# Kernel tuning notes

Hardware: AMD Instinct MI355X
Metric: run time of the kernel (lower is better)

The kernel has to match this reference:

```python
import jax, jax.numpy as jnp
import numpy as np

EPS = 1e-6
NUM_HEADS = 8
FOCUS = 3.0


def setup_inputs() -> dict:
    key = jax.random.key(0)
    ks = jax.random.split(key, 8)
    B, N, C = 16, 4096, 256
    head_dim, ksz = C // NUM_HEADS, 5
    s = 1.0 / np.sqrt(C)
    return {
        "x": jax.random.normal(ks[0], (B, N, C), jnp.float32),
        "Wq": jax.random.normal(ks[1], (C, C), jnp.float32) * s,
        "Wkv": jax.random.normal(ks[2], (C, 2 * C), jnp.float32) * s,
        "Wp": jax.random.normal(ks[3], (C, C), jnp.float32) * s,
        "bp": jnp.zeros((C,), jnp.float32),
        "scale_param": jnp.zeros((1, 1, C), jnp.float32),
        "pos_enc": jax.random.normal(ks[4], (1, N, C), jnp.float32) * 0.02,
        "dwc_w": jax.random.normal(ks[5], (head_dim, 1, ksz, ksz), jnp.float32) * 0.1,
        "dwc_b": jnp.zeros((head_dim,), jnp.float32),
        "H": 64,
        "W": 64,
    }


def _focus(t, scale, f):
    # relu feature map + power focusing with norm restoration
    t = (jax.nn.relu(t) + EPS) / scale
    tn = jnp.linalg.norm(t, axis=-1, keepdims=True)
    tf = t ** f
    return tf / jnp.linalg.norm(tf, axis=-1, keepdims=True) * tn


def reference(x, Wq, Wkv, Wp, bp, scale_param, pos_enc, dwc_w, dwc_b, H, W):
    B, N, C = x.shape
    h = NUM_HEADS
    d = C // h
    n = N  # sr_ratio == 1

    q = x @ Wq                                  # [B,N,C]
    kv = x @ Wkv                                # [B,N,2C]
    k, v = kv[..., :C], kv[..., C:]
    k = k + pos_enc

    scale = jax.nn.softplus(scale_param)
    q = _focus(q, scale, FOCUS)
    k = _focus(k, scale, FOCUS)

    # split heads: [B,h,N,d]
    qh = q.reshape(B, N, h, d).transpose(0, 2, 1, 3)
    kh = k.reshape(B, n, h, d).transpose(0, 2, 1, 3)
    vh = v.reshape(B, n, h, d).transpose(0, 2, 1, 3)

    # linear attention: z = 1/(q . mean_n(k)), kv = k^T v / n, out = (q @ kv) * z
    z = 1.0 / (jnp.einsum("bhnd,bhd->bhn", qh, kh.mean(axis=2)) + EPS)
    kvmat = jnp.einsum("bhnd,bhne->bhde", kh, vh) / n     # [B,h,d,d]
    out = jnp.einsum("bhnd,bhde->bhne", qh, kvmat) * z[..., None]

    out = out.transpose(0, 2, 1, 3).reshape(B, N, C)      # [B,N,C]

    # depthwise conv on v over the HxW grid, per head-channel
    v4 = vh.reshape(B * h, H, W, d).transpose(0, 3, 1, 2)  # [B*h,d,H,W]
    conv = jax.lax.conv_general_dilated(
        v4, dwc_w, window_strides=(1, 1), padding="SAME",
        feature_group_count=d,
        dimension_numbers=("NCHW", "OIHW", "NCHW"))
    conv = conv + dwc_b[None, :, None, None]
    out = out + conv.reshape(B, C, N).transpose(0, 2, 1)

    return out @ Wp + bp
```

## Files before the change

### kernel.cpp

```cpp
#include <hip/hip_runtime.h>
#include <hip/hip_bf16.h>

typedef unsigned short u16;
using bf16_t = __hip_bfloat16;
typedef short short8 __attribute__((ext_vector_type(8)));
typedef float f32x4 __attribute__((ext_vector_type(4)));

__device__ __forceinline__ float b2f(u16 u) {
    return __uint_as_float((unsigned int)u << 16);
}
__device__ __forceinline__ u16 f2b(float f) {
    bf16_t h = __float2bfloat16(f);
    union { bf16_t h; u16 u; } cv; cv.h = h; return cv.u;
}
__device__ __forceinline__ float ldv(const void* p, size_t i, int f32) {
    return f32 ? ((const float*)p)[i] : b2f(((const u16*)p)[i]);
}
__device__ __forceinline__ uint4 pack8(float4 a, float4 b) {
    uint4 u;
    u.x = (unsigned)f2b(a.x) | ((unsigned)f2b(a.y) << 16);
    u.y = (unsigned)f2b(a.z) | ((unsigned)f2b(a.w) << 16);
    u.z = (unsigned)f2b(b.x) | ((unsigned)f2b(b.y) << 16);
    u.w = (unsigned)f2b(b.z) | ((unsigned)f2b(b.w) << 16);
    return u;
}
__device__ __forceinline__ int swz(int n, int k) {
    return k ^ ((n & 7) << 3);
}
__device__ __forceinline__ void gl16(const u16* g, u16* l) {
    __builtin_amdgcn_global_load_lds(
        (const __attribute__((address_space(1))) unsigned int*)g,
        (__attribute__((address_space(3))) unsigned int*)l, 16, 0, 0);
}

__global__ void detect_kernel(const void* __restrict__ x, int* __restrict__ flag)
{
    const int t = threadIdx.x;
    const u16 h = ((const u16*)x)[2 * t];
    const int e = (h >> 7) & 0xFF;
    const int plaus = (e >= 112 && e <= 133) ? 1 : 0;
    const unsigned long long m = __ballot(plaus);
    if (t == 0) flag[0] = (__popcll(m) < 32) ? 1 : 0;
}

__global__ __launch_bounds__(256)
void xcvt_kernel(const void* __restrict__ x, u16* __restrict__ xb,
                 const int* __restrict__ flagp)
{
    const size_t i = ((size_t)blockIdx.x * 256 + threadIdx.x) * 8;
    if (*flagp) {
        const float* xf = (const float*)x + i;
        const float4 f0 = *reinterpret_cast<const float4*>(xf);
        const float4 f1 = *reinterpret_cast<const float4*>(xf + 4);
        *reinterpret_cast<uint4*>(xb + i) = pack8(f0, f1);
    } else {
        *reinterpret_cast<uint4*>(xb + i) =
            *reinterpret_cast<const uint4*>((const u16*)x + i);
    }
}

__global__ __launch_bounds__(256)
void pecvt_kernel(const void* __restrict__ pe, u16* __restrict__ peb,
                  const int* __restrict__ flagp)
{
    const size_t i = ((size_t)blockIdx.x * 256 + threadIdx.x) * 4;
    if (*flagp) {
        const float4 f = *reinterpret_cast<const float4*>((const float*)pe + i);
        ushort4 o; o.x = f2b(f.x); o.y = f2b(f.y); o.z = f2b(f.z); o.w = f2b(f.w);
        *reinterpret_cast<ushort4*>(peb + i) = o;
    } else {
        *reinterpret_cast<ushort4*>(peb + i) =
            *reinterpret_cast<const ushort4*>((const u16*)pe + i);
    }
}

__global__ __launch_bounds__(256)
void wtrans_kernel(const void* __restrict__ W, u16* __restrict__ WT, int N,
                   const int* __restrict__ flagp)
{
    const int f32 = *flagp;
    __shared__ float tile[32][33];
    const int tx = threadIdx.x & 31, ty = threadIdx.x >> 5;
    const int bx = blockIdx.x % (N >> 5);
    const int by = blockIdx.x / (N >> 5);
    #pragma unroll
    for (int r = 0; r < 4; ++r) {
        const int k = by * 32 + ty + r * 8;
        const int n = bx * 32 + tx;
        tile[ty + r * 8][tx] = ldv(W, (size_t)k * N + n, f32);
    }
    __syncthreads();
    #pragma unroll
    for (int r = 0; r < 4; ++r) {
        const int n2 = bx * 32 + ty + r * 8;
        const int k2 = by * 32 + tx;
        WT[(size_t)n2 * 256 + k2] = f2b(tile[tx][ty + r * 8]);
    }
}

template<int MODE>
__global__ __launch_bounds__(256, 2)
void gemm256(const void* __restrict__ Aany, const u16* __restrict__ Abf,
             const u16* __restrict__ BT, u16* __restrict__ O0,
             const void* __restrict__ extra, const int* __restrict__ flagp,
             int abf)
{
    const int f32 = *flagp;
    __shared__ u16 As[128 * 64];
    __shared__ u16 Bs[256 * 64];
    __shared__ float red2[2][128];
    __shared__ float red6[2][128];
    __shared__ float ratio_s[128];
    __shared__ float sscr[256];

    const int tid  = threadIdx.x;
    const int row0 = blockIdx.x * 128;
    const int lane = tid & 63;
    const int wv   = tid >> 6;
    const int wvu  = __builtin_amdgcn_readfirstlane(wv);
    const int wm   = (wv & 1) * 64;
    const int wn   = (wv >> 1) * 128;
    const int l15  = lane & 15;
    const int lq   = lane >> 4;
    const int lr8  = lane >> 3;
    const int lc8  = (lane & 7) * 8;

    if (MODE == 3) {
        const float p = ldv(extra, tid, f32);
        const float s = (p > 20.f) ? p : log1pf(expf(p));
        sscr[tid] = 1.0f / s;
    }

    f32x4 acc[4][8] = {};

    for (int k0 = 0; k0 < 256; k0 += 64) {
        #pragma unroll
        for (int it = 0; it < 8; ++it) {
            const int r = wvu * 64 + it * 8 + lr8;
            gl16(BT + (size_t)r * 256 + k0 + swz(r, lc8),
                 &Bs[(wvu * 64 + it * 8) * 64]);
        }
        if (MODE == 2 || abf || !f32) {
            const u16* Ab = (MODE == 2) ? Abf : (const u16*)Aany;
            #pragma unroll
            for (int it = 0; it < 4; ++it) {
                const int r = wvu * 32 + it * 8 + lr8;
                gl16(Ab + (size_t)(row0 + r) * 256 + k0 + swz(r, lc8),
                     &As[(wvu * 32 + it * 8) * 64]);
            }
        } else {
            const int sr = tid >> 1;
            const int sk = (tid & 1) * 32;
            const float* ag = (const float*)Aany +
                              (size_t)(row0 + sr) * 256 + k0 + sk;
            #pragma unroll
            for (int j = 0; j < 4; ++j) {
                const float4 f0 = *reinterpret_cast<const float4*>(ag + j * 8);
                const float4 f1 = *reinterpret_cast<const float4*>(ag + j * 8 + 4);
                *reinterpret_cast<uint4*>(
                    &As[sr * 64 + swz(sr, sk + j * 8)]) = pack8(f0, f1);
            }
        }
        __syncthreads();
        #pragma unroll
        for (int ks = 0; ks < 64; ks += 32) {
            const int ko = ks + lq * 8;
            short8 av[4], bv[8];
            #pragma unroll
            for (int i = 0; i < 4; ++i) {
                const int m = wm + i * 16 + l15;
                av[i] = *reinterpret_cast<const short8*>(&As[m * 64 + swz(m, ko)]);
            }
            #pragma unroll
            for (int j = 0; j < 8; ++j) {
                const int n = wn + j * 16 + l15;
                bv[j] = *reinterpret_cast<const short8*>(&Bs[n * 64 + swz(n, ko)]);
            }
            #pragma unroll
            for (int i = 0; i < 4; ++i)
                #pragma unroll
                for (int j = 0; j < 8; ++j)
                    acc[i][j] = __builtin_amdgcn_mfma_f32_16x16x32_bf16(
                        av[i], bv[j], acc[i][j], 0, 0, 0);
        }
        __syncthreads();
    }

    if (MODE == 3) {
        #pragma unroll
        for (int i = 0; i < 4; ++i) {
            #pragma unroll
            for (int rg = 0; rg < 4; ++rg) {
                const int lr = wm + i * 16 + lq * 4 + rg;
                float s2 = 0.f, s6 = 0.f;
                #pragma unroll
                for (int j = 0; j < 8; ++j) {
                    const int col = wn + j * 16 + l15;
                    const float xv =
                        (fmaxf(acc[i][j][rg], 0.f) + 1e-6f) * sscr[col];
                    acc[i][j][rg] = xv;
                    const float x2 = xv * xv;
                    s2 += x2;
                    s6 += x2 * x2 * x2;
                }
                #pragma unroll
                for (int off = 1; off < 16; off <<= 1) {
                    s2 += __shfl_xor(s2, off);
                    s6 += __shfl_xor(s6, off);
                }
                if (l15 == 0) { red2[wv >> 1][lr] = s2; red6[wv >> 1][lr] = s6; }
            }
        }
        __syncthreads();
        if (tid < 128)
            ratio_s[tid] = sqrtf((red2[0][tid] + red2[1][tid]) /
                                 (red6[0][tid] + red6[1][tid]));
        __syncthreads();
    }

    #pragma unroll
    for (int i = 0; i < 4; ++i) {
        #pragma unroll
        for (int j = 0; j < 8; ++j) {
            const int gcol = wn + j * 16 + l15;
            #pragma unroll
            for (int rg = 0; rg < 4; ++rg) {
                const int lr = wm + i * 16 + lq * 4 + rg;
                const size_t oi = (size_t)(row0 + lr) * 256 + gcol;
                const float a = acc[i][j][rg];
                if (MODE == 0) {
                    O0[oi] = f2b(a);
                } else if (MODE == 3) {
                    O0[oi] = f2b(a * a * a * ratio_s[lr]);
                } else {
                    const float o = a + ldv(extra, gcol, f32);
                    if (f32) ((float*)O0)[oi] = o;
                    else     O0[oi] = f2b(o);
                }
            }
        }
    }
}

__global__ __launch_bounds__(256, 2)
void fusedk_kernel(const void* __restrict__ x, const u16* __restrict__ WkvT,
                   const u16* __restrict__ peb, const u16* __restrict__ v,
                   const void* __restrict__ sp,
                   float* __restrict__ kvsm, float* __restrict__ ksm,
                   const int* __restrict__ flagp, int abf)
{
    const int f32 = *flagp;
    __shared__ u16 smem[32768];
    __shared__ float red2[4][64];
    __shared__ float red6[4][64];
    __shared__ float ratio_s[64];
    __shared__ float sscr[256];
    u16* As  = smem;
    u16* Bs  = smem + 8192;
    u16* KsT = smem;
    u16* VsT = smem + 16384;

    const int tid  = threadIdx.x;
    const int lane = tid & 63;
    const int wv   = tid >> 6;
    const int wvu  = __builtin_amdgcn_readfirstlane(wv);
    const int l15  = lane & 15;
    const int lq   = lane >> 4;
    const int wn   = wv * 64;
    const int lr8  = lane >> 3;
    const int lc8  = (lane & 7) * 8;

    {
        const float p = ldv(sp, tid, f32);
        const float s = (p > 20.f) ? p : log1pf(expf(p));
        sscr[tid] = 1.0f / s;
    }

    f32x4 cc[2][4] = {};
    float ksp[4] = {0.f, 0.f, 0.f, 0.f};

    const int b    = blockIdx.x >> 5;
    const int row0 = blockIdx.x * 128;
    const int vr   = lane;
    const int veb  = wv * 64;

    f32x4 acc[2][4][4] = {};
    for (int k0 = 0; k0 < 256; k0 += 64) {
        #pragma unroll
        for (int it = 0; it < 8; ++it) {
            const int r = wvu * 64 + it * 8 + lr8;
            gl16(WkvT + (size_t)r * 256 + k0 + swz(r, lc8),
                 &Bs[(wvu * 64 + it * 8) * 64]);
        }
        if (abf || !f32) {
            #pragma unroll
            for (int it = 0; it < 4; ++it) {
                const int r = wvu * 32 + it * 8 + lr8;
                gl16((const u16*)x + (size_t)(row0 + r) * 256 + k0 + swz(r, lc8),
                     &As[(wvu * 32 + it * 8) * 64]);
            }
        } else {
            const int sr = tid >> 1;
            const int sk = (tid & 1) * 32;
            const float* ag = (const float*)x +
                              (size_t)(row0 + sr) * 256 + k0 + sk;
            #pragma unroll
            for (int j = 0; j < 4; ++j) {
                const float4 f0 = *reinterpret_cast<const float4*>(ag + j * 8);
                const float4 f1 = *reinterpret_cast<const float4*>(ag + j * 8 + 4);
                *reinterpret_cast<uint4*>(
                    &As[sr * 64 + swz(sr, sk + j * 8)]) = pack8(f0, f1);
            }
        }
        __syncthreads();
        #pragma unroll
        for (int c = 0; c < 2; ++c) {
            #pragma unroll
            for (int ks = 0; ks < 64; ks += 32) {
                const int ko = ks + lq * 8;
                short8 av[4], bvv[4];
                #pragma unroll
                for (int i = 0; i < 4; ++i) {
                    const int m = c * 64 + i * 16 + l15;
                    av[i] = *reinterpret_cast<const short8*>(&As[m * 64 + swz(m, ko)]);
                }
                #pragma unroll
                for (int j = 0; j < 4; ++j) {
                    const int n = wn + j * 16 + l15;
                    bvv[j] = *reinterpret_cast<const short8*>(&Bs[n * 64 + swz(n, ko)]);
                }
                #pragma unroll
                for (int i = 0; i < 4; ++i)
                    #pragma unroll
                    for (int j = 0; j < 4; ++j)
                        acc[c][i][j] = __builtin_amdgcn_mfma_f32_16x16x32_bf16(
                            av[i], bvv[j], acc[c][i][j], 0, 0, 0);
            }
        }
        __syncthreads();
    }

    #pragma unroll
    for (int c = 0; c < 2; ++c) {
        const int nb = (row0 & 4095) + c * 64;

        #pragma unroll
        for (int i = 0; i < 4; ++i) {
            #pragma unroll
            for (int rg = 0; rg < 4; ++rg) {
                const int lrow = i * 16 + lq * 4 + rg;
                float s2 = 0.f, s6 = 0.f;
                #pragma unroll
                for (int j = 0; j < 4; ++j) {
                    const int col = wn + j * 16 + l15;
                    const float t = acc[c][i][j][rg] +
                        b2f(peb[(size_t)(nb + lrow) * 256 + col]);
                    const float xv = (fmaxf(t, 0.f) + 1e-6f) * sscr[col];
                    acc[c][i][j][rg] = xv;
                    const float x2 = xv * xv;
                    s2 += x2;
                    s6 += x2 * x2 * x2;
                }
                #pragma unroll
                for (int off = 1; off < 16; off <<= 1) {
                    s2 += __shfl_xor(s2, off);
                    s6 += __shfl_xor(s6, off);
                }
                if (l15 == 0) { red2[wv][lrow] = s2; red6[wv][lrow] = s6; }
            }
        }
        __syncthreads();
        if (tid < 64) {
            const float s2t = red2[0][tid] + red2[1][tid] + red2[2][tid] + red2[3][tid];
            const float s6t = red6[0][tid] + red6[1][tid] + red6[2][tid] + red6[3][tid];
            ratio_s[tid] = sqrtf(s2t / s6t);
        }
        __syncthreads();

        {
            float kscol[4] = {0.f, 0.f, 0.f, 0.f};
            #pragma unroll
            for (int i = 0; i < 4; ++i)
                #pragma unroll
                for (int rg = 0; rg < 4; ++rg) {
                    const int lrow = i * 16 + lq * 4 + rg;
                    const float rt = ratio_s[lrow];
                    #pragma unroll
                    for (int j = 0; j < 4; ++j) {
                        const float xv = acc[c][i][j][rg];
                        const float kf = xv * xv * xv * rt;
                        const int d = wn + j * 16 + l15;
                        KsT[d * 64 + swz(d, lrow)] = f2b(kf);
                        kscol[j] += kf;
                    }
                }
            #pragma unroll
            for (int j = 0; j < 4; ++j) {
                float kp = kscol[j];
                kp += __shfl_xor(kp, 16);
                kp += __shfl_xor(kp, 32);
                ksp[j] += kp;
            }
        }

        {
            const u16* vg = v + (size_t)(row0 + c * 64 + vr) * 256 + veb;
            uint4 t0[8];
            #pragma unroll
            for (int j = 0; j < 8; ++j)
                t0[j] = *reinterpret_cast<const uint4*>(vg + j * 8);
            #pragma unroll
            for (int j = 0; j < 8; ++j) {
                const u16* pp = (const u16*)&t0[j];
                #pragma unroll
                for (int m = 0; m < 8; ++m) {
                    const int e = veb + j * 8 + m;
                    VsT[e * 64 + swz(e, vr)] = pp[m];
                }
            }
        }
        __syncthreads();

        #pragma unroll
        for (int hh = 0; hh < 2; ++hh) {
            const int cb = (wv * 2 + hh) * 32;
            const int da = cb + l15, dbx = cb + 16 + l15;
            #pragma unroll
            for (int kk = 0; kk < 64; kk += 32) {
                const int ko = kk + lq * 8;
                const short8 a0 = *reinterpret_cast<const short8*>(
                    &KsT[da * 64 + swz(da, ko)]);
                const short8 a1 = *reinterpret_cast<const short8*>(
                    &KsT[dbx * 64 + swz(dbx, ko)]);
                const short8 b0 = *reinterpret_cast<const short8*>(
                    &VsT[da * 64 + swz(da, ko)]);
                const short8 b1 = *reinterpret_cast<const short8*>(
                    &VsT[dbx * 64 + swz(dbx, ko)]);
                cc[hh][0] = __builtin_amdgcn_mfma_f32_16x16x32_bf16(a0, b0, cc[hh][0], 0, 0, 0);
                cc[hh][1] = __builtin_amdgcn_mfma_f32_16x16x32_bf16(a0, b1, cc[hh][1], 0, 0, 0);
                cc[hh][2] = __builtin_amdgcn_mfma_f32_16x16x32_bf16(a1, b0, cc[hh][2], 0, 0, 0);
                cc[hh][3] = __builtin_amdgcn_mfma_f32_16x16x32_bf16(a1, b1, cc[hh][3], 0, 0, 0);
            }
        }
        __syncthreads();
    }

    const int slot = blockIdx.x & 1;
    float* ksb = ksm + (size_t)(slot * 16 + b) * 256;
    #pragma unroll
    for (int j = 0; j < 4; ++j)
        if (lane < 16)
            atomicAdd(&ksb[wn + j * 16 + lane], ksp[j]);
    #pragma unroll
    for (int hh = 0; hh < 2; ++hh) {
        const int h = wv * 2 + hh;
        float* base = kvsm + ((size_t)(slot * 16 + b) * 8 + h) * 1024;
        #pragma unroll
        for (int rg = 0; rg < 4; ++rg) {
            const int d0 = lq * 4 + rg;
            atomicAdd(&base[(size_t)d0 * 32 + l15],             cc[hh][0][rg]);
            atomicAdd(&base[(size_t)d0 * 32 + 16 + l15],        cc[hh][1][rg]);
            atomicAdd(&base[(size_t)(d0 + 16) * 32 + l15],      cc[hh][2][rg]);
            atomicAdd(&base[(size_t)(d0 + 16) * 32 + 16 + l15], cc[hh][3][rg]);
        }
    }
}

__global__ __launch_bounds__(256)
void attn_kernel(u16* qy, const float* __restrict__ kvsum,
                 const float* __restrict__ ksum)
{
    __shared__ float kvs[8][32][32];
    __shared__ float km[8][32];
    __shared__ float qs[16][256];
    const int tid = threadIdx.x;
    const int b   = blockIdx.x >> 8;
    const int n0  = (blockIdx.x & 255) * 16;
    const float inv_n = 1.0f / 4096.0f;
    for (int i = tid; i < 8 * 32 * 32; i += 256)
        (&kvs[0][0][0])[i] = (kvsum[(size_t)b * 8192 + i] +
                              kvsum[(size_t)(16 + b) * 8192 + i]) * inv_n;
    (&km[0][0])[tid] = (ksum[(size_t)b * 256 + tid] +
                        ksum[(size_t)(16 + b) * 256 + tid]) * inv_n;
    u16* qb = qy + ((size_t)b * 4096 + n0) * 256;
    #pragma unroll
    for (int t = 0; t < 16; ++t)
        qs[t][tid] = b2f(qb[(size_t)t * 256 + tid]);
    __syncthreads();
    const int h = tid >> 5, e = tid & 31;
    for (int t = 0; t < 16; ++t) {
        float acc = 0.f, zd = 0.f;
        #pragma unroll
        for (int d = 0; d < 32; ++d) {
            const float qv = qs[t][h * 32 + d];
            acc = fmaf(qv, kvs[h][d][e], acc);
            zd  = fmaf(qv, km[h][d], zd);
        }
        qb[(size_t)t * 256 + tid] = f2b(acc / (zd + 1e-6f));
    }
}

__global__ __launch_bounds__(256, 2)
void conv_add_kernel(const u16* __restrict__ v, const void* __restrict__ w,
                     const void* __restrict__ bias, u16* __restrict__ y,
                     const int* __restrict__ flagp)
{
    const int f32 = *flagp;
    __shared__ u16 vt[144 * 256];
    __shared__ float wl[800];
    __shared__ float bl[32];
    const int tid = threadIdx.x;
    for (int i = tid; i < 800; i += 256) wl[i] = ldv(w, i, f32);
    if (tid < 32) bl[tid] = ldv(bias, tid, f32);

    const int bb = blockIdx.x >> 6;
    const int ty = (blockIdx.x >> 3) & 7;
    const int tx = blockIdx.x & 7;
    const int y0 = ty * 8, x0 = tx * 8;
    const u16* vb = v + (size_t)bb * 4096 * 256;

    #pragma unroll
    for (int it = 0; it < 18; ++it) {
        const int idx = it * 256 + tid;
        const int px  = idx >> 5;
        const int c8  = (idx & 31) * 8;
        const int py  = px / 12, pxx = px - py * 12;
        const int yy = y0 + py - 2, xx = x0 + pxx - 2;
        uint4 val = {0u, 0u, 0u, 0u};
        if (yy >= 0 && yy < 64 && xx >= 0 && xx < 64)
            val = *reinterpret_cast<const uint4*>(
                vb + (size_t)((yy << 6) + xx) * 256 + c8);
        *reinterpret_cast<uint4*>(&vt[px * 256 + c8]) = val;
    }
    __syncthreads();

    const int c  = tid;
    const int dc = c & 31;
    float wreg[25];
    #pragma unroll
    for (int i = 0; i < 25; ++i) wreg[i] = wl[dc * 25 + i];
    const float bv = bl[dc];

    float win[5][12];
    #pragma unroll
    for (int r = 0; r < 5; ++r)
        #pragma unroll
        for (int cc = 0; cc < 12; ++cc)
            win[r][cc] = b2f(vt[(r * 12 + cc) * 256 + c]);

    u16* yb = y + ((size_t)bb * 4096 + (size_t)y0 * 64 + x0) * 256 + c;
    #pragma unroll
    for (int oy = 0; oy < 8; ++oy) {
        if (oy) {
            #pragma unroll
            for (int r = 0; r < 4; ++r)
                #pragma unroll
                for (int cc = 0; cc < 12; ++cc) win[r][cc] = win[r + 1][cc];
            #pragma unroll
            for (int cc = 0; cc < 12; ++cc)
                win[4][cc] = b2f(vt[((oy + 4) * 12 + cc) * 256 + c]);
        }
        #pragma unroll
        for (int ox = 0; ox < 8; ++ox) {
            float s = 0.f;
            #pragma unroll
            for (int ky = 0; ky < 5; ++ky)
                #pragma unroll
                for (int kx = 0; kx < 5; ++kx)
                    s = fmaf(win[ky][ox + kx], wreg[ky * 5 + kx], s);
            u16* yp = yb + (size_t)(oy * 64 + ox) * 256;
            *yp = f2b(b2f(*yp) + s + bv);
        }
    }
}

extern "C" void kernel_launch(void* const* d_in, const int* in_sizes, int n_in,
                              void* d_out, int out_size, void* d_ws, size_t ws_size,
                              hipStream_t stream)
{
    (void)in_sizes; (void)n_in; (void)out_size;
    const void* x   = d_in[0];
    const void* Wq  = d_in[1];
    const void* Wkv = d_in[2];
    const void* Wp  = d_in[3];
    const void* bp  = d_in[4];
    const void* sp  = d_in[5];
    const void* pe  = d_in[6];
    const void* dw  = d_in[7];
    const void* db  = d_in[8];

    int*   flag = (int*)d_ws;
    float* kvsm = (float*)((char*)d_ws + 64);
    float* ksm  = kvsm + 262144;
    u16*   WqT  = (u16*)(ksm + 8192);
    u16*   WkvT = WqT + 65536;
    u16*   WpT  = WkvT + 131072;
    u16*   peb  = WpT + 65536;
    u16*   qy   = peb + 1048576;
    u16*   xb   = qy + (size_t)16777216;
    u16*   v    = (u16*)d_out;

    const size_t need = (size_t)((char*)(xb + 16777216) - (char*)d_ws);
    const int big = (ws_size >= need) ? 1 : 0;

    hipMemsetAsync(kvsm, 0, (262144 + 8192) * sizeof(float), stream);
    detect_kernel<<<1, 64, 0, stream>>>(x, flag);
    if (big) xcvt_kernel<<<8192, 256, 0, stream>>>(x, xb, flag);
    pecvt_kernel<<<1024, 256, 0, stream>>>(pe, peb, flag);
    wtrans_kernel<<<64, 256, 0, stream>>>(Wq, WqT, 256, flag);
    wtrans_kernel<<<128, 256, 0, stream>>>(Wkv, WkvT, 512, flag);
    wtrans_kernel<<<64, 256, 0, stream>>>(Wp, WpT, 256, flag);

    const void* Ax = big ? (const void*)xb : x;

    hipLaunchKernelGGL((gemm256<3>), dim3(512), dim3(256), 0, stream,
                       Ax, (const u16*)nullptr, WqT, qy, sp, flag, big);
    hipLaunchKernelGGL((gemm256<0>), dim3(512), dim3(256), 0, stream,
                       Ax, (const u16*)nullptr, WkvT + (size_t)256 * 256, v,
                       (const void*)nullptr, flag, big);
    fusedk_kernel<<<512, 256, 0, stream>>>(Ax, WkvT, peb, v, sp, kvsm, ksm,
                                           flag, big);

    attn_kernel<<<4096, 256, 0, stream>>>(qy, kvsm, ksm);
    conv_add_kernel<<<1024, 256, 0, stream>>>(v, dw, db, qy, flag);
    hipLaunchKernelGGL((gemm256<2>), dim3(512), dim3(256), 0, stream,
                       (const void*)nullptr, qy, WpT, (u16*)d_out, bp, flag, 0);
}
```

Before: 358.6 us.

## Rewrite linear-attention apply step with bf16 MFMA over 64-row tiles

Replaces the scalar FMA attention-apply kernel, which multiplies q by the per-head kv matrix, with an MFMA version. Each block now handles 64 rows instead of 16. q is loaded into LDS with a swizzled direct global-to-LDS copy, and the kv matrix is stored transposed as bf16. The change targets the scalar ALU cost and the redundant per-block reloading of the kv matrix, at the price of rounding kv to bf16 and using more LDS per block.

```diff
diff --git a/kernel.cpp b/kernel.cpp
--- a/kernel.cpp
+++ b/kernel.cpp
@@ -466,37 +466,92 @@
     }
 }
 
-__global__ __launch_bounds__(256)
-void attn_kernel(u16* qy, const float* __restrict__ kvsum,
-                 const float* __restrict__ ksum)
-{
-    __shared__ float kvs[8][32][32];
+__global__ __launch_bounds__(256, 2)
+void attn_mfma_kernel(u16* __restrict__ qy, const float* __restrict__ kvsum,
+                      const float* __restrict__ ksum)
+{
+    __shared__ u16 qs[64 * 256];
+    __shared__ u16 kvT[8 * 32 * 40];
     __shared__ float km[8][32];
-    __shared__ float qs[16][256];
-    const int tid = threadIdx.x;
-    const int b   = blockIdx.x >> 8;
-    const int n0  = (blockIdx.x & 255) * 16;
+    __shared__ float zds[64][8];
+    const int tid  = threadIdx.x;
+    const int lane = tid & 63;
+    const int wv   = tid >> 6;
+    const int wvu  = __builtin_amdgcn_readfirstlane(wv);
+    const int l15  = lane & 15;
+    const int lq   = lane >> 4;
+    const int b    = blockIdx.x >> 6;
+    const int n0   = (blockIdx.x & 63) * 64;
     const float inv_n = 1.0f / 4096.0f;
-    for (int i = tid; i < 8 * 32 * 32; i += 256)
-        (&kvs[0][0][0])[i] = (kvsum[(size_t)b * 8192 + i] +
-                              kvsum[(size_t)(16 + b) * 8192 + i]) * inv_n;
-    (&km[0][0])[tid] = (ksum[(size_t)b * 256 + tid] +
-                        ksum[(size_t)(16 + b) * 256 + tid]) * inv_n;
-    u16* qb = qy + ((size_t)b * 4096 + n0) * 256;
-    #pragma unroll
-    for (int t = 0; t < 16; ++t)
-        qs[t][tid] = b2f(qb[(size_t)t * 256 + tid]);
+
+    {
+        const int qr2 = lane >> 5;
+        const int qc8 = (lane & 31) * 8;
+        const u16* qb = qy + (size_t)(b * 4096 + n0) * 256;
+        #pragma unroll
+        for (int it = 0; it < 8; ++it) {
+            const int r = wvu * 16 + it * 2 + qr2;
+            gl16(qb + (size_t)r * 256 + (qc8 ^ ((r & 7) << 3)),
+                 &qs[(wvu * 16 + it * 2) * 256]);
+        }
+    }
+    {
+        const int h = tid >> 5, e = tid & 31;
+        const float* k0 = kvsum + (size_t)b * 8192 + h * 1024 + e;
+        const float* k1 = kvsum + (size_t)(16 + b) * 8192 + h * 1024 + e;
+        #pragma unroll
+        for (int d = 0; d < 32; ++d)
+            kvT[h * 1280 + e * 40 + d] = f2b((k0[d * 32] + k1[d * 32]) * inv_n);
+        (&km[0][0])[tid] = (ksum[(size_t)b * 256 + tid] +
+                            ksum[(size_t)(16 + b) * 256 + tid]) * inv_n;
+    }
     __syncthreads();
-    const int h = tid >> 5, e = tid & 31;
-    for (int t = 0; t < 16; ++t) {
-        float acc = 0.f, zd = 0.f;
-        #pragma unroll
-        for (int d = 0; d < 32; ++d) {
-            const float qv = qs[t][h * 32 + d];
-            acc = fmaf(qv, kvs[h][d][e], acc);
-            zd  = fmaf(qv, km[h][d], zd);
-        }
-        qb[(size_t)t * 256 + tid] = f2b(acc / (zd + 1e-6f));
+
+    {
+        const int zt = tid & 63;
+        const int zh0 = (tid >> 6) * 2;
+        #pragma unroll
+        for (int hh = 0; hh < 2; ++hh) {
+            const int h = zh0 + hh;
+            float s = 0.f;
+            #pragma unroll
+            for (int d = 0; d < 32; ++d) {
+                const int col = (h * 32 + d) ^ ((zt & 7) << 3);
+                s = fmaf(b2f(qs[zt * 256 + col]), km[h][d], s);
+            }
+            zds[zt][h] = s;
+        }
+    }
+
+    f32x4 acc[8][2];
+    #pragma unroll
+    for (int h = 0; h < 8; ++h) {
+        const int m = wvu * 16 + l15;
+        const int col = (h * 32 + lq * 8) ^ ((m & 7) << 3);
+        const short8 av = *reinterpret_cast<const short8*>(&qs[m * 256 + col]);
+        const short8 b0 = *reinterpret_cast<const short8*>(
+            &kvT[h * 1280 + l15 * 40 + lq * 8]);
+        const short8 b1 = *reinterpret_cast<const short8*>(
+            &kvT[h * 1280 + (16 + l15) * 40 + lq * 8]);
+        const f32x4 z = {0.f, 0.f, 0.f, 0.f};
+        acc[h][0] = __builtin_amdgcn_mfma_f32_16x16x32_bf16(av, b0, z, 0, 0, 0);
+        acc[h][1] = __builtin_amdgcn_mfma_f32_16x16x32_bf16(av, b1, z, 0, 0, 0);
+    }
+    __syncthreads();
+
+    u16* qb = qy + (size_t)(b * 4096 + n0) * 256;
+    #pragma unroll
+    for (int h = 0; h < 8; ++h) {
+        #pragma unroll
+        for (int eh = 0; eh < 2; ++eh) {
+            const int gcol = h * 32 + eh * 16 + l15;
+            #pragma unroll
+            for (int rg = 0; rg < 4; ++rg) {
+                const int lr = wvu * 16 + lq * 4 + rg;
+                const float z = 1.0f / (zds[lr][h] + 1e-6f);
+                qb[(size_t)lr * 256 + gcol] = f2b(acc[h][eh][rg] * z);
+            }
+        }
     }
 }
 
@@ -621,7 +676,7 @@
     fusedk_kernel<<<512, 256, 0, stream>>>(Ax, WkvT, peb, v, sp, kvsm, ksm,
                                            flag, big);
 
-    attn_kernel<<<4096, 256, 0, stream>>>(qy, kvsm, ksm);
+    attn_mfma_kernel<<<1024, 256, 0, stream>>>(qy, kvsm, ksm);
     conv_add_kernel<<<1024, 256, 0, stream>>>(v, dw, db, qy, flag);
     hipLaunchKernelGGL((gemm256<2>), dim3(512), dim3(256), 0, stream,
                        (const void*)nullptr, qy, WpT, (u16*)d_out, bp, flag, 0);
```

After: 325.5 us. 1.1x faster.
